# Kernel tuning notes

Measured on AMD Instinct MI355X. Metric: run time of the kernel, lower is better.

Reference implementation:

```python
import jax, jax.numpy as jnp
import numpy as np

N = 100000          # num_nodes
E = 1600000         # num_edges (avg degree 16)
FEAT = 16           # z-embedding dim
IN_DIM = FEAT + 4   # + 4 physics scalars
HID = 128           # hidden_dim
NUM_LAYERS = 2
NUM_REL = 3
NUM_TYPES = 4
LN_EPS = 1e-5


def setup_inputs() -> dict:
    key = jax.random.key(0)
    ks = jax.random.split(key, 20)
    s = 0.05
    return {
        "z": jax.random.randint(ks[0], (N,), 0, 100),
        "sd": jax.random.normal(ks[1], (N, 1), jnp.float32),
        "df": jax.random.normal(ks[2], (N, 1), jnp.float32),
        "cond": jax.random.normal(ks[3], (N, 1), jnp.float32),
        "mult": jax.random.normal(ks[4], (N, 1), jnp.float32),
        "node_type": jax.random.randint(ks[5], (N,), 0, NUM_TYPES),
        "edge_index": jax.random.randint(ks[6], (2, E), 0, N),
        "edge_type": jax.random.randint(ks[7], (E,), 0, NUM_REL),
        # parameters
        "z_embed": jax.random.normal(ks[8], (100, FEAT), jnp.float32) * s,
        "enc_W1": jax.random.normal(ks[9], (NUM_TYPES, IN_DIM, HID), jnp.float32) * s,
        "enc_b1": jnp.zeros((NUM_TYPES, HID), jnp.float32),
        "enc_W2": jax.random.normal(ks[10], (NUM_TYPES, HID, HID), jnp.float32) * s,
        "enc_b2": jnp.zeros((NUM_TYPES, HID), jnp.float32),
        "lin_W": jax.random.normal(ks[11], (NUM_LAYERS, HID, HID), jnp.float32) * s,
        "lin_b": jnp.zeros((NUM_LAYERS, HID), jnp.float32),
        "rel_W": jax.random.normal(ks[12], (NUM_LAYERS, NUM_REL, HID, HID), jnp.float32) * s,
        "ln_g": jnp.ones((NUM_LAYERS, HID), jnp.float32),
        "ln_b": jnp.zeros((NUM_LAYERS, HID), jnp.float32),
        "reg_W": jax.random.normal(ks[13], (HID, 1), jnp.float32) * s,
        "reg_b": jnp.zeros((1,), jnp.float32),
    }


def reference(z, sd, df, cond, mult, node_type, edge_index, edge_type,
              z_embed, enc_W1, enc_b1, enc_W2, enc_b2,
              lin_W, lin_b, rel_W, ln_g, ln_b, reg_W, reg_b):
    # FeatureBuilder: [z embedding | 4 physics scalars] -> [N, IN_DIM]
    raw = jnp.concatenate([z_embed[z], sd, df, cond, mult], axis=1)
    n = raw.shape[0]

    # TypeSpecificEncoder: per-node-type 2-layer MLP, selected by node_type
    x = jnp.zeros((n, enc_W2.shape[-1]), raw.dtype)
    for t in range(enc_W1.shape[0]):
        h = jax.nn.relu(raw @ enc_W1[t] + enc_b1[t]) @ enc_W2[t] + enc_b2[t]
        x = jnp.where((node_type == t)[:, None], h, x)

    src, dst = edge_index[0], edge_index[1]
    # degree over ALL edges (as in the torch code), clamped to >= 1
    deg = jax.ops.segment_sum(jnp.ones(src.shape[0], x.dtype), dst, num_segments=n)
    deg = jnp.clip(deg, 1.0)[:, None]

    # stacked MultiRelationGNNLayer: gather -> per-relation matmul -> scatter-add
    for l in range(lin_W.shape[0]):
        xs = x[src]                               # [E, HID] gather
        msg = jnp.zeros_like(xs)
        for r in range(rel_W.shape[1]):
            mask_r = (edge_type == r)[:, None].astype(x.dtype)
            msg = msg + (xs @ rel_W[l, r]) * mask_r
        agg = jax.ops.segment_sum(msg, dst, num_segments=n) / deg
        h = x @ lin_W[l] + lin_b[l] + agg
        # LayerNorm
        mu = jnp.mean(h, axis=-1, keepdims=True)
        var = jnp.mean((h - mu) ** 2, axis=-1, keepdims=True)
        x = (h - mu) / jnp.sqrt(var + LN_EPS) * ln_g[l] + ln_b[l]

    pooled = jnp.mean(x, axis=0)                  # [HID]
    return pooled @ reg_W + reg_b                 # [1]
```

## Files before the change

### kernel.cpp

```cpp
#include <hip/hip_runtime.h>

#define NN 100000
#define NE 1600000
#define HD 128
#define IND 20
#define LNEPS 1e-5f
#define NLIST2 400000
#define NBKT 3125
#define PASSA_B 256
#define EDGES_PER_B 6250
#define FILL_B 256
#define WCAT_B 512
#define WCATE_B 256
#define W1P_B 128
#define FILLN_B 400
#define ENC_B 12500
#define NWIN 2
#define WINB 1563
#define ASTRIDE 260
#define SORT_CAP 4096
#define PAD_PER_BKT 672
#define NEP (NE + NBKT * PAD_PER_BKT)
#define H1S 136
#define AES 72

typedef unsigned int uint32;
typedef unsigned short ushort16;
typedef __attribute__((ext_vector_type(8))) short bf16x8;
typedef __attribute__((ext_vector_type(4))) float f32x4;
typedef __attribute__((ext_vector_type(2))) float f32x2;

__device__ __forceinline__ ushort16 f2bf(float f) {
    uint32 u = __float_as_uint(f);
    u += 0x7fffu + ((u >> 16) & 1u);
    return (ushort16)(u >> 16);
}
__device__ __forceinline__ float bf2f1(ushort16 h) {
    return __uint_as_float(((uint32)h) << 16);
}
__device__ __forceinline__ uint32 pack2bf(float2 v) {
    return (uint32)f2bf(v.x) | ((uint32)f2bf(v.y) << 16);
}


__global__ __launch_bounds__(256) void k_hist(const int* __restrict__ ei,
                                              const int* __restrict__ et,
                                              int* __restrict__ H,
                                              ushort16* __restrict__ key16,
                                              unsigned* __restrict__ hdr32,
                                              const float* __restrict__ W2,
                                              ushort16* __restrict__ Weh,
                                              ushort16* __restrict__ Wel,
                                              const float* __restrict__ W1,
                                              ushort16* __restrict__ W1e,
                                              const int* __restrict__ nt,
                                              int* misc, unsigned* nodelist,
                                              uint32* x0, uint32* x1) {
    __shared__ int hist[NBKT];
    int bid = blockIdx.x, tid = threadIdx.x;

    if (bid >= PASSA_B + WCATE_B + W1P_B) {
        int rb = bid - PASSA_B - WCATE_B - W1P_B;
        int i = rb * 256 + tid;
        int st = FILLN_B * 256;
        int lane = tid & 63;
        if (rb == 0 && tid < 32) {
            x0[(size_t)NN * 32 + tid] = 0;
            x1[(size_t)NN * 32 + tid] = 0;
        }
        for (int n = i; n < NN; n += st) {
            int t = nt[n];
#pragma unroll
            for (int tt = 0; tt < 4; tt++) {
                unsigned long long m = __ballot(t == tt);
                if (t == tt) {
                    int leader = __ffsll((unsigned long long)m) - 1;
                    int base = 0;
                    if (lane == leader) base = atomicAdd(&misc[8 + tt], (int)__popcll(m));
                    base = __shfl(base, leader);
                    int prefix = (int)__popcll(m & (((unsigned long long)1 << lane) - 1));
                    nodelist[tt * NN + base + prefix] = (unsigned)n | ((unsigned)tt << 17);
                }
            }
        }
        return;
    }
    if (bid >= PASSA_B + WCATE_B) {
        int idx = (bid - PASSA_B - WCATE_B) * 256 + tid;
        int jj = idx & 7;
        int lane = (idx >> 3) & 63;
        int ntile = (idx >> 9) & 7;
        int kstep = (idx >> 12) & 1;
        int t = (idx >> 13) & 3;
        int ke = kstep * 32 + ((lane >> 4) * 8) + jj;
        int n = ntile * 16 + (lane & 15);
        float w = 0.f;
        int sel = 0;
        if (ke < 60) {
            int k0 = ke / 3;
            sel = ke - 3 * k0;
            w = W1[((size_t)t * IND + k0) * HD + n];
        }
        ushort16 hi = f2bf(w);
        W1e[idx] = (sel == 2) ? f2bf(w - bf2f1(hi)) : hi;
        return;
    }
    if (bid >= PASSA_B) {
        int idx = (bid - PASSA_B) * 256 + tid;
        int jj = idx & 7;
        int lane = (idx >> 3) & 63;
        int ntile = (idx >> 9) & 7;
        int kt = (idx >> 12) & 3;
        int t = (idx >> 14) & 3;
        int k = kt * 32 + ((lane >> 4) * 8) + jj;
        int n = ntile * 16 + (lane & 15);
        float v = W2[((size_t)t * HD + k) * HD + n];
        ushort16 hi = f2bf(v);
        Weh[idx] = hi;
        Wel[idx] = f2bf(v - bf2f1(hi));
        return;
    }

    for (int k = tid; k < NBKT; k += 256) hist[k] = 0;
    __syncthreads();
    int e0 = bid * EDGES_PER_B, e1 = e0 + EDGES_PER_B;
    for (int e = e0 + tid; e < e1; e += 256) {
        int d = ei[NE + e];
        int s = ei[e];
        int r = et[e];
        int bkt = d >> 5;
        key16[e] = (ushort16)bkt;
        hdr32[e] = (unsigned)s | ((unsigned)r << 17) | ((unsigned)(d & 31) << 19);
        atomicAdd(&hist[bkt], 1);
    }
    __syncthreads();
    for (int k = tid; k < NBKT; k += 256) H[bid * NBKT + k] = hist[k];
}


__global__ __launch_bounds__(256) void k_s1(int* __restrict__ H, int* __restrict__ btot) {
    int bkt = blockIdx.x * 256 + threadIdx.x;
    if (bkt >= NBKT) return;
    int run = 0;
    for (int jm = 0; jm < PASSA_B; jm += 8) {
        int t0 = H[(jm + 0) * NBKT + bkt];
        int t1 = H[(jm + 1) * NBKT + bkt];
        int t2 = H[(jm + 2) * NBKT + bkt];
        int t3 = H[(jm + 3) * NBKT + bkt];
        int t4 = H[(jm + 4) * NBKT + bkt];
        int t5 = H[(jm + 5) * NBKT + bkt];
        int t6 = H[(jm + 6) * NBKT + bkt];
        int t7 = H[(jm + 7) * NBKT + bkt];
        H[(jm + 0) * NBKT + bkt] = run; run += t0;
        H[(jm + 1) * NBKT + bkt] = run; run += t1;
        H[(jm + 2) * NBKT + bkt] = run; run += t2;
        H[(jm + 3) * NBKT + bkt] = run; run += t3;
        H[(jm + 4) * NBKT + bkt] = run; run += t4;
        H[(jm + 5) * NBKT + bkt] = run; run += t5;
        H[(jm + 6) * NBKT + bkt] = run; run += t6;
        H[(jm + 7) * NBKT + bkt] = run; run += t7;
    }
    btot[bkt] = run;
}

__global__ __launch_bounds__(1024) void k_s2(const int* __restrict__ btot,
                                             int* __restrict__ boff) {
    __shared__ int s[1024];
    int t = threadIdx.x;
    int v4[4];
    int sum = 0;
#pragma unroll
    for (int i = 0; i < 4; i++) {
        int idx = t * 4 + i;
        v4[i] = (idx < NBKT) ? btot[idx] : 0;
        sum += v4[i];
    }
    s[t] = sum;
    __syncthreads();
    for (int o = 1; o < 1024; o <<= 1) {
        int tv = (t >= o) ? s[t - o] : 0;
        __syncthreads();
        s[t] += tv;
        __syncthreads();
    }
    int run = s[t] - sum;
#pragma unroll
    for (int i = 0; i < 4; i++) {
        int idx = t * 4 + i;
        if (idx < NBKT) boff[idx] = run;
        run += v4[i];
    }
    if (t == 1023) boff[NBKT] = NE;
}


__global__ __launch_bounds__(256) void k_fill2(
        const ushort16* __restrict__ key16, const unsigned* __restrict__ hdr32,
        const int* __restrict__ H, const int* __restrict__ boff,
        unsigned* __restrict__ packed,
        const unsigned* __restrict__ nodelist, const int* __restrict__ z,
        const float* __restrict__ sd, const float* __restrict__ df,
        const float* __restrict__ cond, const float* __restrict__ mult,
        const float* __restrict__ z_embed,
        const ushort16* __restrict__ W1e, const float* __restrict__ b1,
        const float* __restrict__ b2,
        unsigned char* __restrict__ xout,
        const float* __restrict__ rel_W, const float* __restrict__ lin_W,
        ushort16* __restrict__ Wbh, ushort16* __restrict__ Wbl,
        const ushort16* __restrict__ Weh, const ushort16* __restrict__ Wel) {
    __shared__ __attribute__((aligned(16))) char smem[13440];
    int bid = blockIdx.x;
    int tid = threadIdx.x;

    if (bid < FILL_B) {
        int* cur = (int*)smem;
        int e0 = bid * EDGES_PER_B, e1 = e0 + EDGES_PER_B;
        for (int w = 0; w < NWIN; w++) {
            int lo = w * WINB;
            for (int k = tid; k < WINB; k += 256) {
                int bkt = lo + k;
                cur[k] = (bkt < NBKT) ? (boff[bkt] + H[bid * NBKT + bkt]) : 0;
            }
            __syncthreads();
            for (int e = e0 + tid; e < e1; e += 256) {
                int kb = (int)key16[e];
                unsigned d = (unsigned)(kb - lo);
                if (d < (unsigned)WINB) {
                    int p = atomicAdd(&cur[d], 1);
                    packed[p] = hdr32[e];
                }
            }
            __syncthreads();
        }
        return;
    }
    int j = bid - FILL_B;
    if (j < WCAT_B) {
        int idx = j * 256 + tid;
        int jj = idx & 7;
        int lane = (idx >> 3) & 63;
        int ntile = (idx >> 9) & 7;
        int kt = (idx >> 12) & 15;
        int l = (idx >> 16) & 1;
        int k = kt * 32 + ((lane >> 4) * 8) + jj;
        int n = ntile * 16 + (lane & 15);
        float v;
        if (k < 384) v = rel_W[((l * 3 + (k >> 7)) * HD + (k & 127)) * HD + n];
        else         v = lin_W[(l * HD + (k - 384)) * HD + n];
        ushort16 hi = f2bf(v);
        Wbh[idx] = hi;
        Wbl[idx] = f2bf(v - bf2f1(hi));
        return;
    }
    j -= WCAT_B;
    if (j >= ENC_B) return;

    ushort16* Ae  = (ushort16*)smem;
    ushort16* h1b = (ushort16*)(smem + 4608);
    unsigned* ent = (unsigned*)(smem + 4608 + 8704);

    int base = j * 32;
    if (tid < 32) ent[tid] = nodelist[base + tid];
    if (tid >= 64 && tid < 128) {
        int r = (tid - 64) >> 1, c = 30 + (tid & 1);
        ((uint32*)Ae)[r * 36 + c] = 0;
    }
    __syncthreads();
    if (ent[0] == 0xFFFFFFFFu) return;
    int type = (int)(ent[0] >> 17);

    for (int idx = tid; idx < 32 * 20; idx += 256) {
        int nl = idx / 20, f = idx - nl * 20;
        unsigned e = ent[nl];
        float v = 0.f;
        if (e != 0xFFFFFFFFu) {
            int node = (int)(e & 0x1FFFF);
            if (f < 16)      v = z_embed[z[node] * 16 + f];
            else if (f == 16) v = sd[node];
            else if (f == 17) v = df[node];
            else if (f == 18) v = cond[node];
            else              v = mult[node];
        }
        ushort16 hi = f2bf(v);
        ushort16 lo = f2bf(v - bf2f1(hi));
        ushort16* ap = Ae + nl * AES + 3 * f;
        ap[0] = hi; ap[1] = lo; ap[2] = hi;
    }
    __syncthreads();

    int lane = tid & 63, wv = tid >> 6;
    int nt0 = 2 * wv, nt1 = 2 * wv + 1;
    int mrow0 = lane & 15, mrow1 = 16 + (lane & 15);
    int koff = (lane >> 4) * 8;

    {
        f32x4 e00 = {0.f, 0.f, 0.f, 0.f}, e01 = e00, e10 = e00, e11 = e00;
        const bf16x8* w1p = (const bf16x8*)(W1e + (size_t)type * 8192);
#pragma unroll
        for (int ks = 0; ks < 2; ks++) {
            bf16x8 af0 = *(const bf16x8*)&Ae[mrow0 * AES + ks * 32 + koff];
            bf16x8 af1 = *(const bf16x8*)&Ae[mrow1 * AES + ks * 32 + koff];
            bf16x8 bf0 = w1p[(ks * 8 + nt0) * 64 + lane];
            bf16x8 bf1 = w1p[(ks * 8 + nt1) * 64 + lane];
            e00 = __builtin_amdgcn_mfma_f32_16x16x32_bf16(af0, bf0, e00, 0, 0, 0);
            e01 = __builtin_amdgcn_mfma_f32_16x16x32_bf16(af0, bf1, e01, 0, 0, 0);
            e10 = __builtin_amdgcn_mfma_f32_16x16x32_bf16(af1, bf0, e10, 0, 0, 0);
            e11 = __builtin_amdgcn_mfma_f32_16x16x32_bf16(af1, bf1, e11, 0, 0, 0);
        }
        int c0 = nt0 * 16 + (lane & 15), c1 = nt1 * 16 + (lane & 15);
        float bb0 = b1[type * HD + c0], bb1 = b1[type * HD + c1];
        int rb2 = (lane >> 4) * 4;
#pragma unroll
        for (int r = 0; r < 4; r++) {
            h1b[(rb2 + r) * H1S + c0]      = f2bf(fmaxf(e00[r] + bb0, 0.f));
            h1b[(rb2 + r) * H1S + c1]      = f2bf(fmaxf(e01[r] + bb1, 0.f));
            h1b[(16 + rb2 + r) * H1S + c0] = f2bf(fmaxf(e10[r] + bb0, 0.f));
            h1b[(16 + rb2 + r) * H1S + c1] = f2bf(fmaxf(e11[r] + bb1, 0.f));
        }
    }
    __syncthreads();

    f32x4 a00 = {0.f, 0.f, 0.f, 0.f}, a01 = a00, a10 = a00, a11 = a00;
    const bf16x8* weh = (const bf16x8*)(Weh + (size_t)type * 16384);
    const bf16x8* wel = (const bf16x8*)(Wel + (size_t)type * 16384);
    const ushort16* h1p = h1b;
#pragma unroll
    for (int kt = 0; kt < 4; kt++) {
        bf16x8 af0 = *(const bf16x8*)&h1p[mrow0 * H1S + kt * 32 + koff];
        bf16x8 af1 = *(const bf16x8*)&h1p[mrow1 * H1S + kt * 32 + koff];
        bf16x8 bh0 = weh[(kt * 8 + nt0) * 64 + lane];
        bf16x8 bh1 = weh[(kt * 8 + nt1) * 64 + lane];
        bf16x8 bl0 = wel[(kt * 8 + nt0) * 64 + lane];
        bf16x8 bl1 = wel[(kt * 8 + nt1) * 64 + lane];
        a00 = __builtin_amdgcn_mfma_f32_16x16x32_bf16(af0, bh0, a00, 0, 0, 0);
        a01 = __builtin_amdgcn_mfma_f32_16x16x32_bf16(af0, bh1, a01, 0, 0, 0);
        a10 = __builtin_amdgcn_mfma_f32_16x16x32_bf16(af1, bh0, a10, 0, 0, 0);
        a11 = __builtin_amdgcn_mfma_f32_16x16x32_bf16(af1, bh1, a11, 0, 0, 0);
        a00 = __builtin_amdgcn_mfma_f32_16x16x32_bf16(af0, bl0, a00, 0, 0, 0);
        a01 = __builtin_amdgcn_mfma_f32_16x16x32_bf16(af0, bl1, a01, 0, 0, 0);
        a10 = __builtin_amdgcn_mfma_f32_16x16x32_bf16(af1, bl0, a10, 0, 0, 0);
        a11 = __builtin_amdgcn_mfma_f32_16x16x32_bf16(af1, bl1, a11, 0, 0, 0);
    }
    int c0 = nt0 * 16 + (lane & 15), c1 = nt1 * 16 + (lane & 15);
    float b20 = b2[type * HD + c0], b21 = b2[type * HD + c1];
    int rb = (lane >> 4) * 4;
#pragma unroll
    for (int r = 0; r < 4; r++) {
        int r0 = rb + r, r1 = 16 + rb + r;
        unsigned e0v = ent[r0], e1v = ent[r1];
        if (e0v != 0xFFFFFFFFu) {
            int node = (int)(e0v & 0x1FFFF);
            int p0 = __builtin_amdgcn_cvt_pk_fp8_f32(a00[r] + b20, a00[r] + b20, 0, false);
            int p1 = __builtin_amdgcn_cvt_pk_fp8_f32(a01[r] + b21, a01[r] + b21, 0, false);
            xout[(size_t)node * HD + c0] = (unsigned char)(p0 & 0xff);
            xout[(size_t)node * HD + c1] = (unsigned char)(p1 & 0xff);
        }
        if (e1v != 0xFFFFFFFFu) {
            int node = (int)(e1v & 0x1FFFF);
            int p0 = __builtin_amdgcn_cvt_pk_fp8_f32(a10[r] + b20, a10[r] + b20, 0, false);
            int p1 = __builtin_amdgcn_cvt_pk_fp8_f32(a11[r] + b21, a11[r] + b21, 0, false);
            xout[(size_t)node * HD + c0] = (unsigned char)(p0 & 0xff);
            xout[(size_t)node * HD + c1] = (unsigned char)(p1 & 0xff);
        }
    }
}


__global__ __launch_bounds__(256) void k_sort2(const unsigned* __restrict__ packed,
                                               const int* __restrict__ boff,
                                               unsigned* __restrict__ packed2,
                                               int* __restrict__ off,
                                               int* __restrict__ degarr) {
    __shared__ unsigned ebuf[SORT_CAP];
    __shared__ int hs[96];
    __shared__ int cur[96];
    __shared__ int segp[97];
    int b = blockIdx.x;
    int tid = threadIdx.x;
    int base = boff[b];
    int tot = boff[b + 1] - base;
    if (tot > SORT_CAP) tot = SORT_CAP;
    int pb = base + PAD_PER_BKT * b;

    if (tid < 96) hs[tid] = 0;
    for (int e = tid; e < tot; e += 256) ebuf[e] = packed[base + e];
    __syncthreads();
    for (int e = tid; e < tot; e += 256) {
        unsigned h = ebuf[e];
        int key = (int)(h >> 19) * 3 + (int)((h >> 17) & 3);
        atomicAdd(&hs[key], 1);
    }
    __syncthreads();
    if (tid == 0) {
        int run = 0;
        for (int k = 0; k < 96; k++) {
            segp[k] = run;
            run += (hs[k] + 7) & ~7;
        }
        segp[96] = run;
    }
    __syncthreads();
    if (tid < 96) {
        cur[tid] = segp[tid];
        off[((b * 32 + tid / 3) << 2) + (tid % 3)] = pb + segp[tid];
    }
    if (tid >= 96 && tid < 128) {
        int n = tid - 96;
        off[((b * 32 + n) << 2) + 3] = pb + segp[3 * n + 3];
        degarr[b * 32 + n] = hs[3 * n] + hs[3 * n + 1] + hs[3 * n + 2];
    }
    __syncthreads();
    for (int e = tid; e < tot; e += 256) {
        unsigned h = ebuf[e];
        int key = (int)(h >> 19) * 3 + (int)((h >> 17) & 3);
        int p = atomicAdd(&cur[key], 1);
        packed2[pb + p] = h & 0x1FFFF;
    }
    __syncthreads();
    if (tid < 96) {
        int e0 = segp[tid] + hs[tid];
        int e1 = segp[tid + 1];
        for (int q = e0; q < e1; q++) packed2[pb + q] = NN;
    }
}


__global__ __launch_bounds__(512, 6) void k_fused(
        const ushort16* __restrict__ x,
        const unsigned* __restrict__ packed,
        const int* __restrict__ off, const int* __restrict__ degarr,
        const ushort16* __restrict__ Wbh, const ushort16* __restrict__ Wbl,
        const float* __restrict__ lb, const float* __restrict__ g,
        const float* __restrict__ bta, unsigned char* __restrict__ xout,
        const float* __restrict__ regW, float* __restrict__ partials) {
    __shared__ uint32 Alds[32 * ASTRIDE];
    __shared__ float stat[32][2];
    __shared__ float red[8];
    int tid = threadIdx.x;
    int lane = tid & 63;
    int wv = tid >> 6;
    int nb = blockIdx.x * 32;

    int bv = off[((nb + wv * 4) << 2) + lane];
    int dgv = degarr[nb + wv * 4 + (lane & 3)];

#pragma unroll
    for (int i = 0; i < 4; i++) {
        int node = nb + wv * 4 + i;
        int bb0 = __builtin_amdgcn_readlane(bv, 4 * i);
        int bb1 = __builtin_amdgcn_readlane(bv, 4 * i + 1);
        int bb2 = __builtin_amdgcn_readlane(bv, 4 * i + 2);
        int bb3 = __builtin_amdgcn_readlane(bv, 4 * i + 3);
        int rdeg = __builtin_amdgcn_readlane(dgv, i);
        float id = 1.0f / (float)(rdeg > 0 ? rdeg : 1);
        int us = x[node * 64 + lane];
        f32x2 a0 = {0.f, 0.f}, a1 = a0, a2 = a0;
        unsigned q0, q1, q2, q3, q4, q5, q6, q7;
        if (bb0 < bb3) {
            q0 = packed[bb0];     q1 = packed[bb0 + 1];
            q2 = packed[bb0 + 2]; q3 = packed[bb0 + 3];
            q4 = packed[bb0 + 4]; q5 = packed[bb0 + 5];
            q6 = packed[bb0 + 6]; q7 = packed[bb0 + 7];
        }
        for (int e = bb0; e < bb3; e += 8) {
            int u0 = x[(int)q0 * 64 + lane];
            int u1 = x[(int)q1 * 64 + lane];
            int u2 = x[(int)q2 * 64 + lane];
            int u3 = x[(int)q3 * 64 + lane];
            int u4 = x[(int)q4 * 64 + lane];
            int u5 = x[(int)q5 * 64 + lane];
            int u6 = x[(int)q6 * 64 + lane];
            int u7 = x[(int)q7 * 64 + lane];
            int en = e + 8;
            unsigned n0 = packed[en];     unsigned n1 = packed[en + 1];
            unsigned n2 = packed[en + 2]; unsigned n3 = packed[en + 3];
            unsigned n4 = packed[en + 4]; unsigned n5 = packed[en + 5];
            unsigned n6 = packed[en + 6]; unsigned n7 = packed[en + 7];
            f32x2 v0 = __builtin_amdgcn_cvt_pk_f32_fp8(u0, false);
            f32x2 v1 = __builtin_amdgcn_cvt_pk_f32_fp8(u1, false);
            f32x2 v2 = __builtin_amdgcn_cvt_pk_f32_fp8(u2, false);
            f32x2 v3 = __builtin_amdgcn_cvt_pk_f32_fp8(u3, false);
            f32x2 v4 = __builtin_amdgcn_cvt_pk_f32_fp8(u4, false);
            f32x2 v5 = __builtin_amdgcn_cvt_pk_f32_fp8(u5, false);
            f32x2 v6 = __builtin_amdgcn_cvt_pk_f32_fp8(u6, false);
            f32x2 v7 = __builtin_amdgcn_cvt_pk_f32_fp8(u7, false);
            f32x2 s = ((v0 + v1) + (v2 + v3)) + ((v4 + v5) + (v6 + v7));
            if (e < bb1)      a0 += s;
            else if (e < bb2) a1 += s;
            else              a2 += s;
            q0 = n0; q1 = n1; q2 = n2; q3 = n3;
            q4 = n4; q5 = n5; q6 = n6; q7 = n7;
        }
        uint32* ar = Alds + (wv * 4 + i) * ASTRIDE;
        float2 s0 = {a0.x * id, a0.y * id};
        float2 s1 = {a1.x * id, a1.y * id};
        float2 s2 = {a2.x * id, a2.y * id};
        f32x2 vs = __builtin_amdgcn_cvt_pk_f32_fp8(us, false);
        float2 s3 = {vs.x, vs.y};
        ar[lane]       = pack2bf(s0);
        ar[64 + lane]  = pack2bf(s1);
        ar[128 + lane] = pack2bf(s2);
        ar[192 + lane] = pack2bf(s3);
    }
    __syncthreads();

    f32x4 acc00 = {0.f, 0.f, 0.f, 0.f}, acc10 = acc00;
    int mrow0 = (lane & 15);
    int mrow1 = 16 + (lane & 15);
    int q4 = (lane >> 4) * 4;
    const bf16x8* wbh = (const bf16x8*)Wbh;
    const bf16x8* wbl = (const bf16x8*)Wbl;

#pragma unroll 4
    for (int kt = 0; kt < 16; kt++) {
        bf16x8 af0 = *(const bf16x8*)&Alds[mrow0 * ASTRIDE + kt * 16 + q4];
        bf16x8 af1 = *(const bf16x8*)&Alds[mrow1 * ASTRIDE + kt * 16 + q4];
        bf16x8 bh0 = wbh[(kt * 8 + wv) * 64 + lane];
        bf16x8 bl0 = wbl[(kt * 8 + wv) * 64 + lane];
        acc00 = __builtin_amdgcn_mfma_f32_16x16x32_bf16(af0, bh0, acc00, 0, 0, 0);
        acc10 = __builtin_amdgcn_mfma_f32_16x16x32_bf16(af1, bh0, acc10, 0, 0, 0);
        acc00 = __builtin_amdgcn_mfma_f32_16x16x32_bf16(af0, bl0, acc00, 0, 0, 0);
        acc10 = __builtin_amdgcn_mfma_f32_16x16x32_bf16(af1, bl0, acc10, 0, 0, 0);
    }
    __syncthreads();

    float* hlds = (float*)Alds;
    int n0 = wv * 16 + (lane & 15);
    float bj0 = lb[n0];
    int rbase = (lane >> 4) * 4;
#pragma unroll
    for (int r = 0; r < 4; r++) {
        hlds[(rbase + r) * 132 + n0]      = acc00[r] + bj0;
        hlds[(16 + rbase + r) * 132 + n0] = acc10[r] + bj0;
    }
    __syncthreads();

    {
        int node = tid >> 4, l16 = tid & 15;
        float s = 0.f, ss = 0.f;
#pragma unroll
        for (int i = 0; i < 8; i++) {
            float v = hlds[node * 132 + l16 + 16 * i];
            s += v; ss += v * v;
        }
        for (int d = 8; d >= 1; d >>= 1) {
            s += __shfl_down(s, d, 16);
            ss += __shfl_down(ss, d, 16);
        }
        if (l16 == 0) {
            float mu = s * (1.f / 128.f);
            float var = ss * (1.f / 128.f) - mu * mu;
            stat[node][0] = mu;
            stat[node][1] = rsqrtf(var + LNEPS);
        }
    }
    __syncthreads();

    {
        int node = tid >> 4, q16 = tid & 15;
        float mu = stat[node][0], rs = stat[node][1];
        const float* hr = hlds + node * 132 + q16 * 8;
        float vv[8];
#pragma unroll
        for (int k = 0; k < 8; k++) {
            int f = q16 * 8 + k;
            vv[k] = (hr[k] - mu) * rs * g[f] + bta[f];
        }
        if (regW == nullptr) {
            int w[2];
#pragma unroll
            for (int p = 0; p < 2; p++) {
                int pk = __builtin_amdgcn_cvt_pk_fp8_f32(vv[p * 4 + 0], vv[p * 4 + 1], 0, false);
                pk = __builtin_amdgcn_cvt_pk_fp8_f32(vv[p * 4 + 2], vv[p * 4 + 3], pk, true);
                w[p] = pk;
            }
            *(int2*)(xout + (size_t)(nb + node) * 128 + q16 * 8) = make_int2(w[0], w[1]);
        } else {
            float s = 0.f;
#pragma unroll
            for (int k = 0; k < 8; k++) s += vv[k] * regW[q16 * 8 + k];
            for (int d = 32; d >= 1; d >>= 1) s += __shfl_down(s, d);
            if (lane == 0) red[wv] = s;
            __syncthreads();
            if (tid == 0) {
                partials[blockIdx.x] = red[0] + red[1] + red[2] + red[3] +
                                       red[4] + red[5] + red[6] + red[7];
            }
        }
    }
}


__global__ __launch_bounds__(1024) void k_red(const float* __restrict__ partials,
                                              const float* __restrict__ reg_b,
                                              float* __restrict__ out) {
    __shared__ float s[16];
    int tid = threadIdx.x;
    float v = 0.f;
    for (int i = tid; i < NBKT; i += 1024) v += partials[i];
    for (int d = 32; d >= 1; d >>= 1) v += __shfl_down(v, d);
    if ((tid & 63) == 0) s[tid >> 6] = v;
    __syncthreads();
    if (tid == 0) {
        float t = 0.f;
#pragma unroll
        for (int i = 0; i < 16; i++) t += s[i];
        out[0] = t * (1.0f / (float)NN) + reg_b[0];
    }
}


extern "C" void kernel_launch(void* const* d_in, const int* in_sizes, int n_in,
                              void* d_out, int out_size, void* d_ws, size_t ws_size,
                              hipStream_t stream) {
    const int*   z       = (const int*)d_in[0];
    const float* sd      = (const float*)d_in[1];
    const float* df      = (const float*)d_in[2];
    const float* cond    = (const float*)d_in[3];
    const float* mult    = (const float*)d_in[4];
    const int*   nt      = (const int*)d_in[5];
    const int*   ei      = (const int*)d_in[6];
    const int*   et      = (const int*)d_in[7];
    const float* z_embed = (const float*)d_in[8];
    const float* enc_W1  = (const float*)d_in[9];
    const float* enc_b1  = (const float*)d_in[10];
    const float* enc_W2  = (const float*)d_in[11];
    const float* enc_b2  = (const float*)d_in[12];
    const float* lin_W   = (const float*)d_in[13];
    const float* lin_b   = (const float*)d_in[14];
    const float* rel_W   = (const float*)d_in[15];
    const float* ln_g    = (const float*)d_in[16];
    const float* ln_b    = (const float*)d_in[17];
    const float* reg_W   = (const float*)d_in[18];
    const float* reg_b   = (const float*)d_in[19];
    float* out = (float*)d_out;

    char* p = (char*)d_ws;
    int* H          = (int*)p;      p += (size_t)PASSA_B * NBKT * 4;
    int* btot       = (int*)p;      p += (size_t)4096 * 4;
    int* boff       = (int*)p;      p += (size_t)4096 * 4;
    int* misc       = (int*)p;      p += 16 * 4;
    float* partials = (float*)p;    p += (size_t)4096 * 4;
    int* off        = (int*)p;      p += (size_t)400384 * 4;
    int* degarr     = (int*)p;      p += (size_t)100096 * 4;
    ushort16* key16 = (ushort16*)p; p += (size_t)NE * 2;
    unsigned* hdr32 = (unsigned*)p; p += (size_t)NE * 4;
    unsigned* packed   = (unsigned*)p; p += (size_t)NE * 4;
    unsigned* packed2  = (unsigned*)p; p += (size_t)(NEP + 16) * 4;
    unsigned* nodelist = (unsigned*)p; p += (size_t)NLIST2 * 4;
    ushort16* Wbh   = (ushort16*)p; p += (size_t)2 * 512 * 128 * 2;
    ushort16* Wbl   = (ushort16*)p; p += (size_t)2 * 512 * 128 * 2;
    ushort16* Weh   = (ushort16*)p; p += (size_t)65536 * 2;
    ushort16* Wel   = (ushort16*)p; p += (size_t)65536 * 2;
    ushort16* W1e   = (ushort16*)p; p += (size_t)32768 * 2;
    unsigned char* x0 = (unsigned char*)p; p += (size_t)(NN + 1) * HD;
    unsigned char* x1 = (unsigned char*)p; p += (size_t)(NN + 1) * HD;

    hipMemsetAsync(misc, 0, 64, stream);
    hipMemsetAsync(nodelist, 0xFF, (size_t)NLIST2 * 4, stream);

    k_hist<<<PASSA_B + WCATE_B + W1P_B + FILLN_B, 256, 0, stream>>>(
        ei, et, H, key16, hdr32, enc_W2, Weh, Wel, enc_W1, W1e,
        nt, misc, nodelist, (uint32*)x0, (uint32*)x1);
    k_s1<<<13, 256, 0, stream>>>(H, btot);
    k_s2<<<1, 1024, 0, stream>>>(btot, boff);
    k_fill2<<<FILL_B + WCAT_B + ENC_B, 256, 0, stream>>>(
        key16, hdr32, H, boff, packed,
        nodelist, z, sd, df, cond, mult, z_embed,
        W1e, enc_b1, enc_b2, x0,
        rel_W, lin_W, Wbh, Wbl, Weh, Wel);
    k_sort2<<<NBKT, 256, 0, stream>>>(packed, boff, packed2, off, degarr);

    k_fused<<<NBKT, 512, 0, stream>>>((const ushort16*)x0, packed2, off, degarr,
                                      Wbh, Wbl,
                                      lin_b, ln_g, ln_b,
                                      x1, nullptr, partials);
    k_fused<<<NBKT, 512, 0, stream>>>((const ushort16*)x1, packed2, off, degarr,
                                      Wbh + (size_t)512 * 128, Wbl + (size_t)512 * 128,
                                      lin_b + HD, ln_g + HD, ln_b + HD,
                                      x0, reg_W, partials);
    k_red<<<1, 1024, 0, stream>>>(partials, reg_b, out);
}
```

Before: 419.0 us.

## Gather two neighbor rows per wave with 4-byte loads, pad segments to 4

The aggregation loop now splits each wave into two halves. Each half gathers a different neighbor row using 32-bit loads that hold four fp8 values, so a wave covers two edges per load instead of one 16-bit load per edge. The two halves' partial sums are combined with a cross-half shuffle before the bf16 pack into LDS. Per-relation segment padding drops from multiples of 8 to multiples of 4, which shrinks the padded edge array and the wasted padding work. In exchange, the unroll depth falls from 8 to 4 outstanding loads per lane, and the kernel adds shuffle overhead.

```diff
diff --git a/kernel.cpp b/kernel.cpp
--- a/kernel.cpp
+++ b/kernel.cpp
@@ -19,7 +19,7 @@
 #define WINB 1563
 #define ASTRIDE 260
 #define SORT_CAP 4096
-#define PAD_PER_BKT 672
+#define PAD_PER_BKT 288
 #define NEP (NE + NBKT * PAD_PER_BKT)
 #define H1S 136
 #define AES 72
@@ -395,7 +395,7 @@
         int run = 0;
         for (int k = 0; k < 96; k++) {
             segp[k] = run;
-            run += (hs[k] + 7) & ~7;
+            run += (hs[k] + 3) & ~3;
         }
         segp[96] = run;
     }
@@ -439,7 +439,10 @@
     int tid = threadIdx.x;
     int lane = tid & 63;
     int wv = tid >> 6;
+    int half = lane >> 5;
+    int li = lane & 31;
     int nb = blockIdx.x * 32;
+    const uint32* xw = (const uint32*)x;
 
     int bv = off[((nb + wv * 4) << 2) + lane];
     int dgv = degarr[nb + wv * 4 + (lane & 3)];
@@ -454,53 +457,51 @@
         int rdeg = __builtin_amdgcn_readlane(dgv, i);
         float id = 1.0f / (float)(rdeg > 0 ? rdeg : 1);
         int us = x[node * 64 + lane];
-        f32x2 a0 = {0.f, 0.f}, a1 = a0, a2 = a0;
-        unsigned q0, q1, q2, q3, q4, q5, q6, q7;
+        f32x2 a0l = {0.f, 0.f}, a0h = a0l, a1l = a0l, a1h = a0l, a2l = a0l, a2h = a0l;
+        unsigned q0, q1, q2, q3;
         if (bb0 < bb3) {
             q0 = packed[bb0];     q1 = packed[bb0 + 1];
             q2 = packed[bb0 + 2]; q3 = packed[bb0 + 3];
-            q4 = packed[bb0 + 4]; q5 = packed[bb0 + 5];
-            q6 = packed[bb0 + 6]; q7 = packed[bb0 + 7];
-        }
-        for (int e = bb0; e < bb3; e += 8) {
-            int u0 = x[(int)q0 * 64 + lane];
-            int u1 = x[(int)q1 * 64 + lane];
-            int u2 = x[(int)q2 * 64 + lane];
-            int u3 = x[(int)q3 * 64 + lane];
-            int u4 = x[(int)q4 * 64 + lane];
-            int u5 = x[(int)q5 * 64 + lane];
-            int u6 = x[(int)q6 * 64 + lane];
-            int u7 = x[(int)q7 * 64 + lane];
-            int en = e + 8;
+        }
+        for (int e = bb0; e < bb3; e += 4) {
+            int r01 = half ? (int)q1 : (int)q0;
+            int r23 = half ? (int)q3 : (int)q2;
+            uint32 u01 = xw[r01 * 32 + li];
+            uint32 u23 = xw[r23 * 32 + li];
+            int en = e + 4;
             unsigned n0 = packed[en];     unsigned n1 = packed[en + 1];
             unsigned n2 = packed[en + 2]; unsigned n3 = packed[en + 3];
-            unsigned n4 = packed[en + 4]; unsigned n5 = packed[en + 5];
-            unsigned n6 = packed[en + 6]; unsigned n7 = packed[en + 7];
-            f32x2 v0 = __builtin_amdgcn_cvt_pk_f32_fp8(u0, false);
-            f32x2 v1 = __builtin_amdgcn_cvt_pk_f32_fp8(u1, false);
-            f32x2 v2 = __builtin_amdgcn_cvt_pk_f32_fp8(u2, false);
-            f32x2 v3 = __builtin_amdgcn_cvt_pk_f32_fp8(u3, false);
-            f32x2 v4 = __builtin_amdgcn_cvt_pk_f32_fp8(u4, false);
-            f32x2 v5 = __builtin_amdgcn_cvt_pk_f32_fp8(u5, false);
-            f32x2 v6 = __builtin_amdgcn_cvt_pk_f32_fp8(u6, false);
-            f32x2 v7 = __builtin_amdgcn_cvt_pk_f32_fp8(u7, false);
-            f32x2 s = ((v0 + v1) + (v2 + v3)) + ((v4 + v5) + (v6 + v7));
-            if (e < bb1)      a0 += s;
-            else if (e < bb2) a1 += s;
-            else              a2 += s;
+            f32x2 l0 = __builtin_amdgcn_cvt_pk_f32_fp8(u01, false);
+            f32x2 h0 = __builtin_amdgcn_cvt_pk_f32_fp8(u01, true);
+            f32x2 l1 = __builtin_amdgcn_cvt_pk_f32_fp8(u23, false);
+            f32x2 h1 = __builtin_amdgcn_cvt_pk_f32_fp8(u23, true);
+            f32x2 sl = l0 + l1, sh = h0 + h1;
+            if (e < bb1)      { a0l += sl; a0h += sh; }
+            else if (e < bb2) { a1l += sl; a1h += sh; }
+            else              { a2l += sl; a2h += sh; }
             q0 = n0; q1 = n1; q2 = n2; q3 = n3;
-            q4 = n4; q5 = n5; q6 = n6; q7 = n7;
-        }
+        }
+        a0l.x += __shfl_xor(a0l.x, 32); a0l.y += __shfl_xor(a0l.y, 32);
+        a0h.x += __shfl_xor(a0h.x, 32); a0h.y += __shfl_xor(a0h.y, 32);
+        a1l.x += __shfl_xor(a1l.x, 32); a1l.y += __shfl_xor(a1l.y, 32);
+        a1h.x += __shfl_xor(a1h.x, 32); a1h.y += __shfl_xor(a1h.y, 32);
+        a2l.x += __shfl_xor(a2l.x, 32); a2l.y += __shfl_xor(a2l.y, 32);
+        a2h.x += __shfl_xor(a2h.x, 32); a2h.y += __shfl_xor(a2h.y, 32);
+
         uint32* ar = Alds + (wv * 4 + i) * ASTRIDE;
-        float2 s0 = {a0.x * id, a0.y * id};
-        float2 s1 = {a1.x * id, a1.y * id};
-        float2 s2 = {a2.x * id, a2.y * id};
+        if (lane < 32) {
+            f32x2 w0l = a0l * id, w0h = a0h * id;
+            f32x2 w1l = a1l * id, w1h = a1h * id;
+            f32x2 w2l = a2l * id, w2h = a2h * id;
+            *(int2*)&ar[2 * li] =
+                make_int2(pack2bf(make_float2(w0l.x, w0l.y)), pack2bf(make_float2(w0h.x, w0h.y)));
+            *(int2*)&ar[64 + 2 * li] =
+                make_int2(pack2bf(make_float2(w1l.x, w1l.y)), pack2bf(make_float2(w1h.x, w1h.y)));
+            *(int2*)&ar[128 + 2 * li] =
+                make_int2(pack2bf(make_float2(w2l.x, w2l.y)), pack2bf(make_float2(w2h.x, w2h.y)));
+        }
         f32x2 vs = __builtin_amdgcn_cvt_pk_f32_fp8(us, false);
-        float2 s3 = {vs.x, vs.y};
-        ar[lane]       = pack2bf(s0);
-        ar[64 + lane]  = pack2bf(s1);
-        ar[128 + lane] = pack2bf(s2);
-        ar[192 + lane] = pack2bf(s3);
+        ar[192 + lane] = pack2bf(make_float2(vs.x, vs.y));
     }
     __syncthreads();
 
```

New measurement: 437.8 us. +4.5%, slower.
